# Kernel tuning notes

Hardware: AMD Instinct MI355X
Metric: run time of the kernel (lower is better)

Reference implementation:

```python
import jax, jax.numpy as jnp
import numpy as np

HEADS = 12
DIM_HEAD = 64
SCALE = DIM_HEAD ** -0.5

def setup_inputs() -> dict:
    key = jax.random.key(0)
    k1, k2, k3, k4 = jax.random.split(key, 4)
    dim, inner = 768, HEADS * DIM_HEAD
    x = jax.random.normal(k1, (4, 2048, dim), dtype=jnp.float32)
    w_qkv = jax.random.normal(k2, (dim, 3 * inner), dtype=jnp.float32) * (dim ** -0.5)
    w_out = jax.random.normal(k3, (inner, dim), dtype=jnp.float32) * (inner ** -0.5)
    b_out = jax.random.normal(k4, (dim,), dtype=jnp.float32) * 0.02
    return {"x": x, "w_qkv": w_qkv, "w_out": w_out, "b_out": b_out}

def reference(x, w_qkv, w_out, b_out):
    B, N, _ = x.shape
    qkv = jnp.einsum('bnd,de->bne', x, w_qkv)  # [B,N,3*inner]
    q, k, v = jnp.split(qkv, 3, axis=-1)
    # b n (h d) -> b h n d
    split_heads = lambda t: t.reshape(B, N, HEADS, DIM_HEAD).transpose(0, 2, 1, 3)
    q, k, v = split_heads(q), split_heads(k), split_heads(v)
    dots = jnp.einsum('bhnd,bhmd->bhnm', q, k) * SCALE  # [B,H,N,N]
    attn = jax.nn.softmax(dots, axis=-1)
    out = jnp.einsum('bhnm,bhmd->bhnd', attn, v)
    out = out.transpose(0, 2, 1, 3).reshape(B, N, HEADS * DIM_HEAD)  # b h n d -> b n (h d)
    return jnp.einsum('bne,ed->bnd', out, w_out) + b_out
```

## Files before the change

kernel.cpp:

```cpp
#include <hip/hip_runtime.h>
#include <stdint.h>

typedef unsigned short ushort_t;
typedef __attribute__((ext_vector_type(8))) short short8;
typedef __attribute__((ext_vector_type(4))) float f32x4;
typedef __attribute__((ext_vector_type(2))) uint32_t u32x2;

#define BATCH 4
#define SEQ 2048
#define DMODEL 768
#define NH 12
#define HD 64
#define QKV3 2304
#define NHEADS 48
#define SCALE_Q 0.18033688011112042f

__device__ __forceinline__ ushort_t f2bf(float f) {
    union { float f; uint32_t u; } v; v.f = f;
    uint32_t u = v.u;
    u += 0x7FFF + ((u >> 16) & 1);
    return (ushort_t)(u >> 16);
}

__device__ __forceinline__ uint32_t pack_bf16(float a, float b) {
#if __has_builtin(__builtin_amdgcn_cvt_pk_bf16_f32)
    typedef __attribute__((ext_vector_type(2))) __bf16 bf16x2;
    bf16x2 r = __builtin_amdgcn_cvt_pk_bf16_f32(a, b);
    return __builtin_bit_cast(uint32_t, r);
#else
    return ((uint32_t)f2bf(b) << 16) | (uint32_t)f2bf(a);
#endif
}

typedef __attribute__((address_space(1))) uint32_t as1_u32;
typedef __attribute__((address_space(3))) uint32_t as3_u32;
__device__ __forceinline__ void async16(void* lds, const void* gsrc) {
    __builtin_amdgcn_global_load_lds((as1_u32*)gsrc, (as3_u32*)lds, 16, 0, 0);
}

__device__ __forceinline__ void wait_vm_lgkm0() {
    __builtin_amdgcn_s_waitcnt(0x0070);
}
__device__ __forceinline__ void wait_vm4_lgkm0() {
    __builtin_amdgcn_s_waitcnt(0x0074);
}

__device__ __forceinline__ void swap32(uint32_t& a, uint32_t& b) {
    asm("v_permlane32_swap_b32 %0, %1" : "+v"(a), "+v"(b));
}
__device__ __forceinline__ void swap16(uint32_t& a, uint32_t& b) {
    asm("v_permlane16_swap_b32 %0, %1" : "+v"(a), "+v"(b));
}

__device__ __forceinline__ void transpose_body(
    const float* __restrict__ in, ushort_t* __restrict__ out,
    int R, int C, int r0, int c0, int tid, ushort_t (*t)[72]) {
#pragma unroll
    for (int i = 0; i < 4; i++) {
        int idx = tid + i * 256;
        int row = idx >> 4, c4 = (idx & 15) * 4;
        float4 v = *(const float4*)(in + (size_t)(r0 + row) * C + c0 + c4);
        ushort4 o; o.x = f2bf(v.x); o.y = f2bf(v.y); o.z = f2bf(v.z); o.w = f2bf(v.w);
        *(ushort4*)&t[row][c4] = o;
    }
    __syncthreads();
#pragma unroll
    for (int i = 0; i < 2; i++) {
        int idx = tid + i * 256;
        int oc = idx >> 3, g8 = (idx & 7) * 8;
        ushort_t tmp[8];
#pragma unroll
        for (int e = 0; e < 8; e++) tmp[e] = t[g8 + e][oc];
        *(short8*)(out + (size_t)(c0 + oc) * R + r0 + g8) = *(const short8*)tmp;
    }
}

__global__ __launch_bounds__(256) void prep(
    const float* __restrict__ x, ushort_t* __restrict__ xb,
    const float* __restrict__ w_qkv, ushort_t* __restrict__ wqT,
    const float* __restrict__ w_out, ushort_t* __restrict__ woT) {
    __shared__ ushort_t t[64][72];
    const int b = blockIdx.x, tid = threadIdx.x;
    if (b < 6144) {
        size_t i = (size_t)b * 256 + tid;
        float4 v = *(const float4*)(x + i * 4);
        ushort4 o; o.x = f2bf(v.x); o.y = f2bf(v.y); o.z = f2bf(v.z); o.w = f2bf(v.w);
        *(ushort4*)(xb + i * 4) = o;
    } else if (b < 6144 + 432) {
        int tb = b - 6144;
        int bx = tb % 36, by = tb / 36;
        transpose_body(w_qkv, wqT, DMODEL, QKV3, by * 64, bx * 64, tid, t);
    } else {
        int tb = b - 6576;
        int bx = tb % 12, by = tb / 12;
        transpose_body(w_out, woT, DMODEL, DMODEL, by * 64, bx * 64, tid, t);
    }
}

__global__ __launch_bounds__(256, 4) void gemm_qkv(
    const ushort_t* __restrict__ A, const ushort_t* __restrict__ B,
    ushort_t* __restrict__ qkv, ushort_t* __restrict__ vT) {
    __shared__ ushort_t As[128 * 64];
    __shared__ ushort_t Bs[128 * 64];

    const int tid = threadIdx.x;
    const int m0 = blockIdx.y * 128, n0 = blockIdx.x * 128;
    const int lane = tid & 63, w = tid >> 6;
    const int wm = w >> 1, wn = w & 1;
    const int l16 = lane & 15, quad = lane >> 4;

    f32x4 acc[4][4];
#pragma unroll
    for (int i = 0; i < 4; i++)
#pragma unroll
        for (int j = 0; j < 4; j++) acc[i][j] = (f32x4){0.f, 0.f, 0.f, 0.f};

    int srow[4], scol[4];
#pragma unroll
    for (int j = 0; j < 4; j++) {
        int s = j * 256 + tid;
        srow[j] = s >> 3;
        scol[j] = ((s & 7) ^ (srow[j] & 7)) * 8;
    }
    const int swz0 = (quad ^ (l16 & 7)) * 8;
    const int swz1 = ((4 + quad) ^ (l16 & 7)) * 8;

    for (int kt = 0; kt < DMODEL; kt += 64) {
#pragma unroll
        for (int j = 0; j < 4; j++) {
            async16(&As[(j * 256 + w * 64) * 8],
                    A + (size_t)(m0 + srow[j]) * DMODEL + kt + scol[j]);
            async16(&Bs[(j * 256 + w * 64) * 8],
                    B + (size_t)(n0 + srow[j]) * DMODEL + kt + scol[j]);
        }
        wait_vm_lgkm0();
        __syncthreads();

        short8 a[4][2], b[4][2];
#pragma unroll
        for (int mi = 0; mi < 4; mi++) {
            int r = (wm * 64 + mi * 16 + l16) * 64;
            a[mi][0] = *(const short8*)&As[r + swz0];
            a[mi][1] = *(const short8*)&As[r + swz1];
        }
#pragma unroll
        for (int ni = 0; ni < 4; ni++) {
            int r = (wn * 64 + ni * 16 + l16) * 64;
            b[ni][0] = *(const short8*)&Bs[r + swz0];
            b[ni][1] = *(const short8*)&Bs[r + swz1];
        }
#pragma unroll
        for (int kk = 0; kk < 2; kk++)
#pragma unroll
            for (int mi = 0; mi < 4; mi++)
#pragma unroll
                for (int ni = 0; ni < 4; ni++)
                    acc[mi][ni] = __builtin_amdgcn_mfma_f32_16x16x32_bf16(
                        a[mi][kk], b[ni][kk], acc[mi][ni], 0, 0, 0);
        __syncthreads();
    }

#pragma unroll
    for (int ni = 0; ni < 4; ni++) {
        int nbase = n0 + wn * 64 + ni * 16;
        int which = nbase / DMODEL;
        int rem = nbase - which * DMODEL;
        int h = rem >> 6;
        int d = (rem & 63) + l16;
        if (which == 2) {
#pragma unroll
            for (int mi = 0; mi < 4; mi++) {
                int mg = m0 + wm * 64 + mi * 16 + quad * 4;
                int b_ = mg >> 11, ns = mg & 2047;
                u32x2 pk = {pack_bf16(acc[mi][ni][0], acc[mi][ni][1]),
                            pack_bf16(acc[mi][ni][2], acc[mi][ni][3])};
                *(u32x2*)(vT + ((size_t)(b_ * NH + h) * HD + d) * SEQ + ns) = pk;
            }
        } else {
            float scale = (which == 0) ? SCALE_Q : 1.0f;
#pragma unroll
            for (int mi = 0; mi < 4; mi++) {
#pragma unroll
                for (int r = 0; r < 4; r++) {
                    int mg = m0 + wm * 64 + mi * 16 + quad * 4 + r;
                    int b_ = mg >> 11, ns = mg & 2047;
                    size_t dst = (((size_t)(which * BATCH + b_) * NH + h) * SEQ + ns) * HD + d;
                    qkv[dst] = f2bf(acc[mi][ni][r] * scale);
                }
            }
        }
    }
}

__global__ __launch_bounds__(256, 3) void attn(
    const ushort_t* __restrict__ qkv, const ushort_t* __restrict__ vT,
    ushort_t* __restrict__ ao) {
    __shared__ ushort_t smem[24576];

    const int tid = threadIdx.x;
    const int bid = blockIdx.x;
    const int i = bid >> 3;
    const int bh = (bid & 7) + 8 * (i % 6);
    const int qt = i / 6;
    const int lane = tid & 63, w = tid >> 6;
    const int l16 = lane & 15, quad = lane >> 4;
    const int qh7 = l16 & 7;

    const ushort_t* qh = qkv + (size_t)bh * (SEQ * HD);
    const ushort_t* kh = qkv + (size_t)(NHEADS + bh) * (SEQ * HD);
    const ushort_t* vh = vT + (size_t)bh * (HD * SEQ);

    short8 aq[2][2];
#pragma unroll
    for (int mi = 0; mi < 2; mi++)
#pragma unroll
        for (int kk = 0; kk < 2; kk++) {
            int row = qt * 128 + w * 32 + mi * 16 + l16;
            aq[mi][kk] = *(const short8*)(qh + (size_t)row * HD + kk * 32 + quad * 8);
        }

    short8 ones8;
#pragma unroll
    for (int j = 0; j < 8; j++) ones8[j] = (short)0x3F80;

    f32x4 acc_l[2];
    f32x4 O[4][2];
#pragma unroll
    for (int mi = 0; mi < 2; mi++) acc_l[mi] = (f32x4){0.f, 0.f, 0.f, 0.f};
#pragma unroll
    for (int nd = 0; nd < 4; nd++)
#pragma unroll
        for (int mi = 0; mi < 2; mi++) O[nd][mi] = (f32x4){0.f, 0.f, 0.f, 0.f};

    int srow[2], scol[2];
#pragma unroll
    for (int j = 0; j < 2; j++) {
        int s = j * 256 + tid;
        srow[j] = s >> 3;
        scol[j] = ((s & 7) ^ (srow[j] & 7)) * 8;
    }
    const int swz0 = (quad ^ qh7) * 8;
    const int swz1 = ((4 + quad) ^ qh7) * 8;

    auto stage = [&](int t, int buf) {
        int nb = buf * 8192, j1 = t * 64;
#pragma unroll
        for (int j = 0; j < 2; j++) {
            async16(&smem[nb + (j * 256 + w * 64) * 8],
                    kh + (size_t)(j1 + srow[j]) * HD + scol[j]);
            async16(&smem[nb + 4096 + (j * 256 + w * 64) * 8],
                    vh + (size_t)srow[j] * SEQ + j1 + scol[j]);
        }
    };

    auto compute = [&](const ushort_t* Ks) {
        const ushort_t* Vs = Ks + 4096;
#pragma unroll
        for (int p = 0; p < 2; p++) {
            uint32_t pkv[2][2][2];
#pragma unroll
            for (int sub = 0; sub < 2; sub++) {
                const int ni = p * 2 + sub;
                int r = (ni * 16 + l16) * 64;
                short8 ak0 = *(const short8*)&Ks[r + swz0];
                short8 ak1 = *(const short8*)&Ks[r + swz1];
#pragma unroll
                for (int mi = 0; mi < 2; mi++) {
                    f32x4 s = __builtin_amdgcn_mfma_f32_16x16x32_bf16(
                        ak0, aq[mi][0], (f32x4){0.f, 0.f, 0.f, 0.f}, 0, 0, 0);
                    s = __builtin_amdgcn_mfma_f32_16x16x32_bf16(
                        ak1, aq[mi][1], s, 0, 0, 0);
                    f32x4 pr;
#pragma unroll
                    for (int rr = 0; rr < 4; rr++)
                        pr[rr] = __builtin_amdgcn_exp2f(s[rr]);
                    pkv[sub][mi][0] = pack_bf16(pr[0], pr[1]);
                    pkv[sub][mi][1] = pack_bf16(pr[2], pr[3]);
                }
            }
            short8 bp32[2];
#pragma unroll
            for (int mi = 0; mi < 2; mi++) {
                uint32_t x0 = pkv[0][mi][0], y0 = pkv[1][mi][0];
                uint32_t x1 = pkv[0][mi][1], y1 = pkv[1][mi][1];
                swap32(x0, y0); swap16(x0, y0);
                swap32(x1, y1); swap16(x1, y1);
                union { short8 s; uint32_t u[4]; } bu;
                bu.u[0] = x0; bu.u[1] = x1; bu.u[2] = y0; bu.u[3] = y1;
                bp32[mi] = bu.s;
            }
            __builtin_amdgcn_s_setprio(1);
#pragma unroll
            for (int mi = 0; mi < 2; mi++)
                acc_l[mi] = __builtin_amdgcn_mfma_f32_16x16x32_bf16(
                    ones8, bp32[mi], acc_l[mi], 0, 0, 0);
#pragma unroll
            for (int nd = 0; nd < 4; nd++) {
                int vrow = nd * 16 + l16;
                short8 av = *(const short8*)&Vs[vrow * 64 +
                                                (((p * 4 + quad) ^ qh7) * 8)];
#pragma unroll
                for (int mi = 0; mi < 2; mi++)
                    O[nd][mi] = __builtin_amdgcn_mfma_f32_16x16x32_bf16(
                        av, bp32[mi], O[nd][mi], 0, 0, 0);
            }
            __builtin_amdgcn_s_setprio(0);
        }
    };

    stage(0, 0);
    stage(1, 1);

    const int NT = SEQ / 64;
    for (int t = 0; t < NT - 1; t++) {
        wait_vm4_lgkm0();
        __builtin_amdgcn_s_barrier();
        if (t + 2 < NT) stage(t + 2, (t + 2) % 3);
        compute(smem + (t % 3) * 8192);
    }
    wait_vm_lgkm0();
    __builtin_amdgcn_s_barrier();
    compute(smem + ((NT - 1) % 3) * 8192);

    float inv[2];
#pragma unroll
    for (int mi = 0; mi < 2; mi++)
        inv[mi] = __builtin_amdgcn_rcpf(acc_l[mi][0]);
    __syncthreads();
    ushort_t* Lt = smem;
#pragma unroll
    for (int mi = 0; mi < 2; mi++)
#pragma unroll
        for (int nd = 0; nd < 4; nd++) {
            int row = w * 32 + mi * 16 + l16;
            int col = nd * 16 + quad * 4;
            uint32_t d0 = pack_bf16(O[nd][mi][0] * inv[mi], O[nd][mi][1] * inv[mi]);
            uint32_t d1 = pack_bf16(O[nd][mi][2] * inv[mi], O[nd][mi][3] * inv[mi]);
            *(u32x2*)&Lt[row * 72 + col] = (u32x2){d0, d1};
        }
    __syncthreads();

    const int b_ = bh / NH, h = bh % NH;
#pragma unroll
    for (int i2 = 0; i2 < 4; i2++) {
        int idx = tid + i2 * 256;
        int row = idx >> 3, c8 = (idx & 7) * 8;
        short8 vv = *(const short8*)&Lt[row * 72 + c8];
        *(short8*)(ao + ((size_t)(b_ * SEQ + qt * 128 + row)) * DMODEL +
                   h * HD + c8) = vv;
    }
}

__global__ __launch_bounds__(256, 4) void gemm_out(
    const ushort_t* __restrict__ A, const ushort_t* __restrict__ B,
    const float* __restrict__ bias, float* __restrict__ out) {
    __shared__ ushort_t As[128 * 64];
    __shared__ ushort_t Bs[128 * 64];

    const int tid = threadIdx.x;
    const int m0 = blockIdx.y * 128, n0 = blockIdx.x * 128;
    const int lane = tid & 63, w = tid >> 6;
    const int wm = w >> 1, wn = w & 1;
    const int l16 = lane & 15, quad = lane >> 4;

    f32x4 acc[4][4];
#pragma unroll
    for (int i = 0; i < 4; i++)
#pragma unroll
        for (int j = 0; j < 4; j++) acc[i][j] = (f32x4){0.f, 0.f, 0.f, 0.f};

    int srow[4], scol[4];
#pragma unroll
    for (int j = 0; j < 4; j++) {
        int s = j * 256 + tid;
        srow[j] = s >> 3;
        scol[j] = ((s & 7) ^ (srow[j] & 7)) * 8;
    }
    const int swz0 = (quad ^ (l16 & 7)) * 8;
    const int swz1 = ((4 + quad) ^ (l16 & 7)) * 8;

    for (int kt = 0; kt < DMODEL; kt += 64) {
#pragma unroll
        for (int j = 0; j < 4; j++) {
            async16(&As[(j * 256 + w * 64) * 8],
                    A + (size_t)(m0 + srow[j]) * DMODEL + kt + scol[j]);
            async16(&Bs[(j * 256 + w * 64) * 8],
                    B + (size_t)(n0 + srow[j]) * DMODEL + kt + scol[j]);
        }
        wait_vm_lgkm0();
        __syncthreads();

        short8 a[4][2], b[4][2];
#pragma unroll
        for (int mi = 0; mi < 4; mi++) {
            int r = (wm * 64 + mi * 16 + l16) * 64;
            a[mi][0] = *(const short8*)&As[r + swz0];
            a[mi][1] = *(const short8*)&As[r + swz1];
        }
#pragma unroll
        for (int ni = 0; ni < 4; ni++) {
            int r = (wn * 64 + ni * 16 + l16) * 64;
            b[ni][0] = *(const short8*)&Bs[r + swz0];
            b[ni][1] = *(const short8*)&Bs[r + swz1];
        }
#pragma unroll
        for (int kk = 0; kk < 2; kk++)
#pragma unroll
            for (int mi = 0; mi < 4; mi++)
#pragma unroll
                for (int ni = 0; ni < 4; ni++)
                    acc[mi][ni] = __builtin_amdgcn_mfma_f32_16x16x32_bf16(
                        a[mi][kk], b[ni][kk], acc[mi][ni], 0, 0, 0);
        __syncthreads();
    }

#pragma unroll
    for (int ni = 0; ni < 4; ni++) {
        int ng = n0 + wn * 64 + ni * 16 + l16;
        float bv = bias[ng];
#pragma unroll
        for (int mi = 0; mi < 4; mi++) {
#pragma unroll
            for (int r = 0; r < 4; r++) {
                int mg = m0 + wm * 64 + mi * 16 + quad * 4 + r;
                out[(size_t)mg * DMODEL + ng] = acc[mi][ni][r] + bv;
            }
        }
    }
}

extern "C" void kernel_launch(void* const* d_in, const int* in_sizes, int n_in,
                              void* d_out, int out_size, void* d_ws, size_t ws_size,
                              hipStream_t stream) {
    const float* x     = (const float*)d_in[0];
    const float* w_qkv = (const float*)d_in[1];
    const float* w_out = (const float*)d_in[2];
    const float* b_out = (const float*)d_in[3];
    float* out = (float*)d_out;

    ushort_t* xb  = (ushort_t*)d_ws;
    ushort_t* wqT = xb  + (size_t)8192 * 768;
    ushort_t* woT = wqT + (size_t)QKV3 * 768;
    ushort_t* qkv = woT + (size_t)768 * 768;
    ushort_t* vT  = qkv + (size_t)3 * NHEADS * SEQ * HD;
    ushort_t* ao  = vT  + (size_t)NHEADS * HD * SEQ;

    prep<<<dim3(6720), 256, 0, stream>>>(x, xb, w_qkv, wqT, w_out, woT);

    gemm_qkv<<<dim3(QKV3 / 128, (BATCH * SEQ) / 128), 256, 0, stream>>>(
        xb, wqT, qkv, vT);

    attn<<<dim3(NHEADS * (SEQ / 128)), 256, 0, stream>>>(qkv, vT, ao);

    gemm_out<<<dim3(DMODEL / 128, (BATCH * SEQ) / 128), 256, 0, stream>>>(
        ao, woT, b_out, out);
}
```

Before: 210.0 us.

## Rewrite QKV GEMM with 256x256 tiles, double-buffered async loads and interleaved MFMA phases

```diff
diff --git a/kernel.cpp b/kernel.cpp
--- a/kernel.cpp
+++ b/kernel.cpp
@@ -43,6 +43,12 @@
 }
 __device__ __forceinline__ void wait_vm4_lgkm0() {
     __builtin_amdgcn_s_waitcnt(0x0074);
+}
+__device__ __forceinline__ void wait_vm8_lgkm0() {
+    __builtin_amdgcn_s_waitcnt(0x0078);
+}
+__device__ __forceinline__ void wait_lgkm0_only() {
+    __builtin_amdgcn_s_waitcnt(0xC07F);
 }
 
 __device__ __forceinline__ void swap32(uint32_t& a, uint32_t& b) {
@@ -97,95 +103,150 @@
     }
 }
 
-__global__ __launch_bounds__(256, 4) void gemm_qkv(
+__global__ __launch_bounds__(512, 1) void gemm_qkv(
     const ushort_t* __restrict__ A, const ushort_t* __restrict__ B,
     ushort_t* __restrict__ qkv, ushort_t* __restrict__ vT) {
-    __shared__ ushort_t As[128 * 64];
-    __shared__ ushort_t Bs[128 * 64];
+    __shared__ ushort_t sm[65536];
 
     const int tid = threadIdx.x;
-    const int m0 = blockIdx.y * 128, n0 = blockIdx.x * 128;
-    const int lane = tid & 63, w = tid >> 6;
-    const int wm = w >> 1, wn = w & 1;
+    const int m0 = blockIdx.y * 256, n0 = blockIdx.x * 256;
+    const int lane = tid & 63, wid = tid >> 6;
+    const int wm = wid >> 2, wn = wid & 3;
     const int l16 = lane & 15, quad = lane >> 4;
-
-    f32x4 acc[4][4];
-#pragma unroll
-    for (int i = 0; i < 4; i++)
+    const int lh7 = l16 & 7;
+
+    f32x4 acc[8][4];
+#pragma unroll
+    for (int i = 0; i < 8; i++)
 #pragma unroll
         for (int j = 0; j < 4; j++) acc[i][j] = (f32x4){0.f, 0.f, 0.f, 0.f};
 
     int srow[4], scol[4];
 #pragma unroll
     for (int j = 0; j < 4; j++) {
-        int s = j * 256 + tid;
-        srow[j] = s >> 3;
-        scol[j] = ((s & 7) ^ (srow[j] & 7)) * 8;
-    }
-    const int swz0 = (quad ^ (l16 & 7)) * 8;
-    const int swz1 = ((4 + quad) ^ (l16 & 7)) * 8;
-
-    for (int kt = 0; kt < DMODEL; kt += 64) {
-#pragma unroll
-        for (int j = 0; j < 4; j++) {
-            async16(&As[(j * 256 + w * 64) * 8],
-                    A + (size_t)(m0 + srow[j]) * DMODEL + kt + scol[j]);
-            async16(&Bs[(j * 256 + w * 64) * 8],
-                    B + (size_t)(n0 + srow[j]) * DMODEL + kt + scol[j]);
-        }
-        wait_vm_lgkm0();
-        __syncthreads();
-
-        short8 a[4][2], b[4][2];
-#pragma unroll
-        for (int mi = 0; mi < 4; mi++) {
-            int r = (wm * 64 + mi * 16 + l16) * 64;
-            a[mi][0] = *(const short8*)&As[r + swz0];
-            a[mi][1] = *(const short8*)&As[r + swz1];
-        }
+        int idx = j * 512 + tid;
+        srow[j] = idx >> 3;
+        scol[j] = ((idx & 7) ^ (srow[j] & 7)) * 8;
+    }
+    const int swz0 = (quad ^ lh7) * 8;
+    const int swz1 = ((4 + quad) ^ lh7) * 8;
+
+    auto stage = [&](int kt, int buf) {
+        ushort_t* Ab = sm + buf * 32768;
+        ushort_t* Bb = Ab + 16384;
+#pragma unroll
+        for (int j = 0; j < 4; j++)
+            async16(&Ab[(j * 512 + tid) * 8],
+                    A + (size_t)(m0 + srow[j]) * DMODEL + kt * 64 + scol[j]);
+#pragma unroll
+        for (int j = 0; j < 4; j++)
+            async16(&Bb[(j * 512 + tid) * 8],
+                    B + (size_t)(n0 + srow[j]) * DMODEL + kt * 64 + scol[j]);
+    };
+
+    stage(0, 0);
+    stage(1, 1);
+
+    const int NKT = DMODEL / 64;
+    for (int t = 0; t < NKT; t++) {
+        if (t + 1 < NKT) wait_vm8_lgkm0();
+        else             wait_vm_lgkm0();
+        __builtin_amdgcn_s_barrier();
+
+        const ushort_t* Ab = sm + (t & 1) * 32768;
+        const ushort_t* Bb = Ab + 16384;
+
+        short8 a[4], b0[4], b1[4];
+#pragma unroll
+        for (int ni = 0; ni < 4; ni++)
+            b0[ni] = *(const short8*)&Bb[(wn * 64 + ni * 16 + l16) * 64 + swz0];
+#pragma unroll
+        for (int mi = 0; mi < 4; mi++)
+            a[mi] = *(const short8*)&Ab[(wm * 128 + mi * 16 + l16) * 64 + swz0];
+        __builtin_amdgcn_s_setprio(1);
+#pragma unroll
+        for (int mi = 0; mi < 4; mi++)
+#pragma unroll
+            for (int ni = 0; ni < 4; ni++)
+                acc[mi][ni] = __builtin_amdgcn_mfma_f32_16x16x32_bf16(
+                    a[mi], b0[ni], acc[mi][ni], 0, 0, 0);
+        __builtin_amdgcn_s_setprio(0);
+        __builtin_amdgcn_sched_barrier(0);
+#pragma unroll
+        for (int mi = 0; mi < 4; mi++)
+            a[mi] = *(const short8*)&Ab[(wm * 128 + (mi + 4) * 16 + l16) * 64 + swz0];
+        __builtin_amdgcn_s_setprio(1);
+#pragma unroll
+        for (int mi = 0; mi < 4; mi++)
+#pragma unroll
+            for (int ni = 0; ni < 4; ni++)
+                acc[mi + 4][ni] = __builtin_amdgcn_mfma_f32_16x16x32_bf16(
+                    a[mi], b0[ni], acc[mi + 4][ni], 0, 0, 0);
+        __builtin_amdgcn_s_setprio(0);
+        __builtin_amdgcn_sched_barrier(0);
+#pragma unroll
+        for (int ni = 0; ni < 4; ni++)
+            b1[ni] = *(const short8*)&Bb[(wn * 64 + ni * 16 + l16) * 64 + swz1];
+#pragma unroll
+        for (int mi = 0; mi < 4; mi++)
+            a[mi] = *(const short8*)&Ab[(wm * 128 + mi * 16 + l16) * 64 + swz1];
+        __builtin_amdgcn_s_setprio(1);
+#pragma unroll
+        for (int mi = 0; mi < 4; mi++)
+#pragma unroll
+            for (int ni = 0; ni < 4; ni++)
+                acc[mi][ni] = __builtin_amdgcn_mfma_f32_16x16x32_bf16(
+                    a[mi], b1[ni], acc[mi][ni], 0, 0, 0);
+        __builtin_amdgcn_s_setprio(0);
+        __builtin_amdgcn_sched_barrier(0);
+#pragma unroll
+        for (int mi = 0; mi < 4; mi++)
+            a[mi] = *(const short8*)&Ab[(wm * 128 + (mi + 4) * 16 + l16) * 64 + swz1];
+        wait_lgkm0_only();
+        __builtin_amdgcn_sched_barrier(0);
+        __builtin_amdgcn_s_barrier();
+        if (t + 2 < NKT) stage(t + 2, t & 1);
+        __builtin_amdgcn_s_setprio(1);
+#pragma unroll
+        for (int mi = 0; mi < 4; mi++)
+#pragma unroll
+            for (int ni = 0; ni < 4; ni++)
+                acc[mi + 4][ni] = __builtin_amdgcn_mfma_f32_16x16x32_bf16(
+                    a[mi], b1[ni], acc[mi + 4][ni], 0, 0, 0);
+        __builtin_amdgcn_s_setprio(0);
+    }
+
+    const int which = n0 / DMODEL;
+    if (which == 2) {
 #pragma unroll
         for (int ni = 0; ni < 4; ni++) {
-            int r = (wn * 64 + ni * 16 + l16) * 64;
-            b[ni][0] = *(const short8*)&Bs[r + swz0];
-            b[ni][1] = *(const short8*)&Bs[r + swz1];
-        }
-#pragma unroll
-        for (int kk = 0; kk < 2; kk++)
-#pragma unroll
-            for (int mi = 0; mi < 4; mi++)
-#pragma unroll
-                for (int ni = 0; ni < 4; ni++)
-                    acc[mi][ni] = __builtin_amdgcn_mfma_f32_16x16x32_bf16(
-                        a[mi][kk], b[ni][kk], acc[mi][ni], 0, 0, 0);
-        __syncthreads();
-    }
-
-#pragma unroll
-    for (int ni = 0; ni < 4; ni++) {
-        int nbase = n0 + wn * 64 + ni * 16;
-        int which = nbase / DMODEL;
-        int rem = nbase - which * DMODEL;
-        int h = rem >> 6;
-        int d = (rem & 63) + l16;
-        if (which == 2) {
-#pragma unroll
-            for (int mi = 0; mi < 4; mi++) {
-                int mg = m0 + wm * 64 + mi * 16 + quad * 4;
+            int rem = (n0 - 2 * DMODEL) + wn * 64 + ni * 16;
+            int h = rem >> 6;
+            int d = (rem & 63) + l16;
+#pragma unroll
+            for (int mi = 0; mi < 8; mi++) {
+                int mg = m0 + wm * 128 + mi * 16 + quad * 4;
                 int b_ = mg >> 11, ns = mg & 2047;
                 u32x2 pk = {pack_bf16(acc[mi][ni][0], acc[mi][ni][1]),
                             pack_bf16(acc[mi][ni][2], acc[mi][ni][3])};
                 *(u32x2*)(vT + ((size_t)(b_ * NH + h) * HD + d) * SEQ + ns) = pk;
             }
-        } else {
-            float scale = (which == 0) ? SCALE_Q : 1.0f;
-#pragma unroll
-            for (int mi = 0; mi < 4; mi++) {
+        }
+    } else {
+        const float scale = (which == 0) ? SCALE_Q : 1.0f;
+#pragma unroll
+        for (int ni = 0; ni < 4; ni++) {
+            int rem = (n0 - which * DMODEL) + wn * 64 + ni * 16;
+            int h = rem >> 6;
+            int d = (rem & 63) + l16;
+#pragma unroll
+            for (int mi = 0; mi < 8; mi++) {
 #pragma unroll
                 for (int r = 0; r < 4; r++) {
-                    int mg = m0 + wm * 64 + mi * 16 + quad * 4 + r;
+                    int mg = m0 + wm * 128 + mi * 16 + quad * 4 + r;
                     int b_ = mg >> 11, ns = mg & 2047;
-                    size_t dst = (((size_t)(which * BATCH + b_) * NH + h) * SEQ + ns) * HD + d;
-                    qkv[dst] = f2bf(acc[mi][ni][r] * scale);
+                    qkv[(((size_t)(which * BATCH + b_) * NH + h) * SEQ + ns) * HD + d] =
+                        f2bf(acc[mi][ni][r] * scale);
                 }
             }
         }
@@ -447,7 +508,7 @@
 
     prep<<<dim3(6720), 256, 0, stream>>>(x, xb, w_qkv, wqT, w_out, woT);
 
-    gemm_qkv<<<dim3(QKV3 / 128, (BATCH * SEQ) / 128), 256, 0, stream>>>(
+    gemm_qkv<<<dim3(QKV3 / 256, (BATCH * SEQ) / 256), 512, 0, stream>>>(
         xb, wqT, qkv, vT);
 
     attn<<<dim3(NHEADS * (SEQ / 128)), 256, 0, stream>>>(qkv, vT, ao);
```

Result: slower. 221.5 us (+5.5%).
